# Optimization experiments

Hardware: AMD Instinct MI355X
Metric: run time of the kernel (lower is better)

The kernel has to match this reference:

```python
import jax, jax.numpy as jnp
import numpy as np
from jax import lax

FX, FY = 518.857, 519.469   # NYU-v2 depth intrinsics (cx/cy unused by forward)
B, H, W = 8, 479, 639       # TRAIN_CROP_SIZE = [W, H]; H+1, W+1 divisible by 4
P = 8                       # even PATCH_SIZE -> box-filter output is [H+1, W+1]
EPS = 1e-6


def _coords():
    # u_u0 = x - W/2, v_v0 = y - H/2, broadcast over [B,1,H,W]
    u = jnp.arange(W, dtype=jnp.float32)[None, None, None, :] - W / 2.0
    v = jnp.arange(H, dtype=jnp.float32)[None, None, :, None] - H / 2.0
    return u, v


def _surface_normal(xyz):
    # xyz: [H, W, 3] -> normals [H, W, 3]
    x, y, z = xyz[..., 0], xyz[..., 1], xyz[..., 2]
    # 9 box-filtered moments in a single depthwise conv (the original does 9 conv2d calls)
    mom = jnp.stack([x * x, x * y, x * z, y * y, y * z, z * z, x, y, z], 0)[None]  # [1,9,H,W]
    kern = jnp.ones((9, 1, P, P), xyz.dtype)
    s = lax.conv_general_dilated(mom, kern, (1, 1), [(P // 2, P // 2)] * 2,
                                 feature_group_count=9)[0]  # [9, H+1, W+1]
    xx, xy, xz, yy, yz, zz, xs, ys, zs = s
    ATA = jnp.stack([xx, xy, xz, xy, yy, yz, xz, yz, zz], -1)  # [H+1, W+1, 9]
    Hp, Wp = ATA.shape[0], ATA.shape[1]
    ATA = ATA.reshape(Hp, Wp, 3, 3) + EPS * jnp.eye(3, dtype=xyz.dtype)
    AT1 = jnp.stack([xs, ys, zs], -1)[..., None]  # [H+1, W+1, 3, 1]
    # original loops over 4x4 sub-patches with overlap=0 -> equivalent full-grid solve
    n = jnp.linalg.solve(ATA, AT1)                # [H+1, W+1, 3, 1]
    n = n / jnp.sqrt(jnp.sum(n * n, axis=2, keepdims=True))
    n = n[:-1, :-1, :, 0]                         # [H, W, 3]
    # orient toward camera: flip where dot(n, xyz) > 0
    flip = jnp.sum(n * xyz, axis=2, keepdims=True) > 0
    return jnp.where(flip, -n, n)


def _fit_normals(depth):
    # depth: [B,1,H,W] -> surface normals [B,3,H,W], zeroed where depth <= 0
    u, v = _coords()
    x = u * depth / FX
    y = v * depth / FY
    xyz = jnp.concatenate([x, y, depth], 1).transpose(0, 2, 3, 1)  # [B,H,W,3]
    sn = jax.vmap(_surface_normal)(xyz).transpose(0, 3, 1, 2)      # [B,3,H,W]
    return jnp.where(depth > 0, sn, 0.0)


def setup_inputs() -> dict:
    key = jax.random.key(0)
    k1, k2 = jax.random.split(key)
    prediction = jax.random.uniform(k1, (B, 1, H, W), jnp.float32)
    gt = jax.random.uniform(k2, (B, 1, H, W), jnp.float32)
    return {"prediction": prediction, "gt": gt}


def reference(prediction, gt):
    return jnp.mean(jnp.abs(_fit_normals(prediction) - _fit_normals(gt)))
```

## Files before the change

kernel.cpp:

```cpp
#include <hip/hip_runtime.h>

#define HH 479
#define WW 639
#define BATCH 8
#define NBLK (20 * 30 * 8)


__device__ __forceinline__ void solve_normal(
    float xx, float xy, float xz, float yy, float yz, float zz,
    float xs, float ys, float zs,
    float a_c, float b_c, float d0,
    float* nx, float* ny, float* nz)
{
    const float EPSV = 1e-6f;
    const float inv64 = 1.0f / 64.0f;
    float hx = xs * inv64, hy = ys * inv64, hz = zs * inv64;
    float cxx = fmaf(-hx, xs, xx) + EPSV;
    float cxy = fmaf(-hx, ys, xy);
    float cxz = fmaf(-hx, zs, xz);
    float cyy = fmaf(-hy, ys, yy) + EPSV;
    float cyz = fmaf(-hy, zs, yz);
    float czz = fmaf(-hz, zs, zz) + EPSV;
    float c00 = fmaf(cyy, czz, -cyz * cyz);
    float c01 = fmaf(cxz, cyz, -cxy * czz);
    float c02 = fmaf(cxy, cyz, -cxz * cyy);
    float c11 = fmaf(cxx, czz, -cxz * cxz);
    float c12 = fmaf(cxy, cxz, -cxx * cyz);
    float c22 = fmaf(cxx, cyy, -cxy * cxy);
    float m0 = fmaf(c00, xs, fmaf(c01, ys, c02 * zs));
    float m1 = fmaf(c01, xs, fmaf(c11, ys, c12 * zs));
    float m2 = fmaf(c02, xs, fmaf(c12, ys, c22 * zs));
    float g  = fmaf(m0, a_c, fmaf(m1, b_c, m2));
    float inv = rsqrtf(fmaf(m0, m0, fmaf(m1, m1, m2 * m2)));
    if (g > 0.0f) inv = -inv;
    if (!(d0 > 0.0f)) inv = 0.0f;
    *nx = m0 * inv; *ny = m1 * inv; *nz = m2 * inv;
}

__global__ __launch_bounds__(256, 8)
void ppal_main(const float* __restrict__ pred, const float* __restrict__ gt,
               double* __restrict__ acc)
{
    const int tx = threadIdx.x;
    const int ty = threadIdx.y;
    const int tid = ty * 16 + tx;
    const int j0 = blockIdx.x * 32;
    const int i0 = blockIdx.y * 16;
    const int b  = blockIdx.z;

    const float invFX = 1.0f / 518.857f;
    const float invFY = 1.0f / 519.469f;

    __shared__ float sd[2][23 * 41];
    __shared__ float4 cs4[624];
    __shared__ float  csTb[624];
    __shared__ float  wsum[4];

    const float* src0 = pred + (size_t)b * (HH * WW);
    const float* src1 = gt   + (size_t)b * (HH * WW);
    for (int idx = tid; idx < 23 * 41; idx += 256) {
        int lr = idx / 41, lc = idx - lr * 41;
        int r = i0 - 4 + lr, c = j0 - 4 + lc;
        bool ok = (lc < 39) && (r >= 0) && (r < HH) && (c >= 0) && (c < WW);
        int off = r * WW + c;
        sd[0][idx] = ok ? src0[off] : 0.0f;
        sd[1][idx] = ok ? src1[off] : 0.0f;
    }

    float aw[9];
#pragma unroll
    for (int m = 0; m < 9; ++m)
        aw[m] = ((float)(j0 + 2 * tx + m - 4) - 319.5f) * invFX;
    const float bc = ((float)(i0 + ty) - 239.5f) * invFY;
    const int ebase = ty * 39 + 2 * tx;

    float n0A[3], n1A[3];
    float contrib = 0.0f;

    __syncthreads();

#pragma unroll
    for (int k = 0; k < 2; ++k) {
        if (tid < 156) {
            int g = tid / 39;
            int c = tid - 39 * g;
            int rb = 4 * g;
            const float* col = &sd[k][c];
            float bv = ((float)(i0 + rb - 4) - 239.5f) * invFY;
            float S1 = 0.f, Sb = 0.f, Sbb = 0.f, T1 = 0.f, Tb = 0.f;
#pragma unroll
            for (int r = 0; r < 8; ++r) {
                float d  = col[(rb + r) * 41];
                float bvr = fmaf((float)r, invFY, bv);
                float bd = bvr * d;
                T1 += d;  Tb += bd;
                S1  = fmaf(d,  d,  S1);
                Sb  = fmaf(bd, d,  Sb);
                Sbb = fmaf(bd, bd, Sbb);
            }
            int e = rb * 39 + c;
            cs4[e]  = make_float4(S1, Sb, Sbb, T1);
            csTb[e] = Tb;
#pragma unroll
            for (int s = 1; s < 4; ++s) {
                float d0 = col[(rb + s - 1) * 41];
                float d1 = col[(rb + s + 7) * 41];
                float b0 = fmaf((float)(s - 1), invFY, bv);
                float b1 = fmaf((float)(s + 7), invFY, bv);
                float bd0 = b0 * d0, bd1 = b1 * d1;
                T1 += d1 - d0;
                Tb += bd1 - bd0;
                S1  += fmaf(d1,  d1,  -d0  * d0);
                Sb  += fmaf(bd1, d1,  -bd0 * d0);
                Sbb += fmaf(bd1, bd1, -bd0 * bd0);
                e += 39;
                cs4[e]  = make_float4(S1, Sb, Sbb, T1);
                csTb[e] = Tb;
            }
        }
        __syncthreads();

        {
            float Sxx = 0.f, Sxy = 0.f, Sxz = 0.f, Syy = 0.f, Syz = 0.f;
            float Szz = 0.f, Sxs = 0.f, Sys = 0.f, Szs = 0.f;
#pragma unroll
            for (int m = 1; m < 8; ++m) {
                int e = ebase + m;
                float4 r = cs4[e];
                float  tb = csTb[e];
                Szz += r.x;  Syz += r.y;  Syy += r.z;
                Szs += r.w;  Sys += tb;
                Sxz = fmaf(aw[m],         r.x, Sxz);
                Sxy = fmaf(aw[m],         r.y, Sxy);
                Sxs = fmaf(aw[m],         r.w, Sxs);
                Sxx = fmaf(aw[m] * aw[m], r.x, Sxx);
            }

            float nn[2][3];
#pragma unroll
            for (int p = 0; p < 2; ++p) {
                int m = (p == 0) ? 0 : 8;
                int e = ebase + m;
                float4 r = cs4[e];
                float  tb = csTb[e];
                float xx = fmaf(aw[m] * aw[m], r.x, Sxx);
                float xy = fmaf(aw[m], r.y, Sxy);
                float xz = fmaf(aw[m], r.x, Sxz);
                float yy = Syy + r.z;
                float yz = Syz + r.y;
                float zz = Szz + r.x;
                float xs = fmaf(aw[m], r.w, Sxs);
                float ys = Sys + tb;
                float zs = Szs + r.w;
                float d0 = sd[k][(ty + 4) * 41 + (2 * tx + p + 4)];
                solve_normal(xx, xy, xz, yy, yz, zz, xs, ys, zs,
                             aw[4 + p], bc, d0, &nn[p][0], &nn[p][1], &nn[p][2]);
            }
            if (k == 0) {
                n0A[0] = nn[0][0]; n0A[1] = nn[0][1]; n0A[2] = nn[0][2];
                n1A[0] = nn[1][0]; n1A[1] = nn[1][1]; n1A[2] = nn[1][2];
                __syncthreads();
            } else {
                const int i = i0 + ty;
                const bool valid0 = (i < HH);
                const bool valid1 = (i < HH) && (j0 + 2 * tx + 1 < WW);
                float c0 = fabsf(n0A[0] - nn[0][0]) + fabsf(n0A[1] - nn[0][1])
                         + fabsf(n0A[2] - nn[0][2]);
                float c1 = fabsf(n1A[0] - nn[1][0]) + fabsf(n1A[1] - nn[1][1])
                         + fabsf(n1A[2] - nn[1][2]);
                contrib = (valid0 ? c0 : 0.0f) + (valid1 ? c1 : 0.0f);
            }
        }
    }

    float v = contrib;
#pragma unroll
    for (int off = 32; off > 0; off >>= 1) v += __shfl_down(v, off, 64);
    int wid = tid >> 6, lane = tid & 63;
    if (lane == 0) wsum[wid] = v;
    __syncthreads();
    if (tid == 0) {
        double bs = (double)wsum[0] + (double)wsum[1] + (double)wsum[2] + (double)wsum[3];
        int slot = blockIdx.x + 20 * blockIdx.y + 600 * blockIdx.z;
        acc[slot] = bs;
    }
}

__global__ void ppal_finalize(const double* __restrict__ acc, float* __restrict__ out)
{
    int tid = threadIdx.x;
    double v = 0.0;
    for (int s = tid; s < NBLK; s += 256) v += acc[s];
#pragma unroll
    for (int off = 32; off > 0; off >>= 1) v += __shfl_down(v, off, 64);
    __shared__ double wsum[4];
    int wid = tid >> 6, lane = tid & 63;
    if (lane == 0) wsum[wid] = v;
    __syncthreads();
    if (tid == 0)
        out[0] = (float)((wsum[0] + wsum[1] + wsum[2] + wsum[3])
                         * (1.0 / 7345944.0));
}

extern "C" void kernel_launch(void* const* d_in, const int* in_sizes, int n_in,
                              void* d_out, int out_size, void* d_ws, size_t ws_size,
                              hipStream_t stream)
{
    const float* pred = (const float*)d_in[0];
    const float* gt   = (const float*)d_in[1];
    float* out  = (float*)d_out;
    double* acc = (double*)d_ws;

    dim3 grid(20, 30, BATCH);
    dim3 block(16, 16);
    ppal_main<<<grid, block, 0, stream>>>(pred, gt, acc);
    ppal_finalize<<<1, 256, 0, stream>>>(acc, out);
}
```

Measured before the change: 98.24 us.

## Process prediction and ground truth together with doubled shared buffers

```diff
diff --git a/kernel.cpp b/kernel.cpp
--- a/kernel.cpp
+++ b/kernel.cpp
@@ -37,7 +37,7 @@
     *nx = m0 * inv; *ny = m1 * inv; *nz = m2 * inv;
 }
 
-__global__ __launch_bounds__(256, 8)
+__global__ __launch_bounds__(256, 4)
 void ppal_main(const float* __restrict__ pred, const float* __restrict__ gt,
                double* __restrict__ acc)
 {
@@ -52,8 +52,8 @@
     const float invFY = 1.0f / 519.469f;
 
     __shared__ float sd[2][23 * 41];
-    __shared__ float4 cs4[624];
-    __shared__ float  csTb[624];
+    __shared__ float4 cs4[2][624];
+    __shared__ float  csTb[2][624];
     __shared__ float  wsum[4];
 
     const float* src0 = pred + (size_t)b * (HH * WW);
@@ -74,102 +74,127 @@
     const float bc = ((float)(i0 + ty) - 239.5f) * invFY;
     const int ebase = ty * 39 + 2 * tx;
 
-    float n0A[3], n1A[3];
+    __syncthreads();
+
+    if (tid < 156) {
+        int g = tid / 39;
+        int c = tid - 39 * g;
+        int rb = 4 * g;
+        const float* colA = &sd[0][c];
+        const float* colB = &sd[1][c];
+        float bv = ((float)(i0 + rb - 4) - 239.5f) * invFY;
+        float SA1 = 0.f, SAb = 0.f, SAbb = 0.f, TA1 = 0.f, TAb = 0.f;
+        float SB1 = 0.f, SBb = 0.f, SBbb = 0.f, TB1 = 0.f, TBb = 0.f;
+#pragma unroll
+        for (int r = 0; r < 8; ++r) {
+            int ro = (rb + r) * 41;
+            float bvr = fmaf((float)r, invFY, bv);
+            float dA = colA[ro], dB = colB[ro];
+            float bdA = bvr * dA, bdB = bvr * dB;
+            TA1 += dA;  TAb += bdA;
+            SA1  = fmaf(dA,  dA,  SA1);
+            SAb  = fmaf(bdA, dA,  SAb);
+            SAbb = fmaf(bdA, bdA, SAbb);
+            TB1 += dB;  TBb += bdB;
+            SB1  = fmaf(dB,  dB,  SB1);
+            SBb  = fmaf(bdB, dB,  SBb);
+            SBbb = fmaf(bdB, bdB, SBbb);
+        }
+        int e = rb * 39 + c;
+        cs4[0][e]  = make_float4(SA1, SAb, SAbb, TA1);
+        csTb[0][e] = TAb;
+        cs4[1][e]  = make_float4(SB1, SBb, SBbb, TB1);
+        csTb[1][e] = TBb;
+#pragma unroll
+        for (int s = 1; s < 4; ++s) {
+            int o0 = (rb + s - 1) * 41, o1 = (rb + s + 7) * 41;
+            float b0 = fmaf((float)(s - 1), invFY, bv);
+            float b1 = fmaf((float)(s + 7), invFY, bv);
+            float d0A = colA[o0], d1A = colA[o1];
+            float d0B = colB[o0], d1B = colB[o1];
+            float bd0A = b0 * d0A, bd1A = b1 * d1A;
+            float bd0B = b0 * d0B, bd1B = b1 * d1B;
+            TA1 += d1A - d0A;
+            TAb += bd1A - bd0A;
+            SA1  += fmaf(d1A,  d1A,  -d0A  * d0A);
+            SAb  += fmaf(bd1A, d1A,  -bd0A * d0A);
+            SAbb += fmaf(bd1A, bd1A, -bd0A * bd0A);
+            TB1 += d1B - d0B;
+            TBb += bd1B - bd0B;
+            SB1  += fmaf(d1B,  d1B,  -d0B  * d0B);
+            SBb  += fmaf(bd1B, d1B,  -bd0B * d0B);
+            SBbb += fmaf(bd1B, bd1B, -bd0B * bd0B);
+            e += 39;
+            cs4[0][e]  = make_float4(SA1, SAb, SAbb, TA1);
+            csTb[0][e] = TAb;
+            cs4[1][e]  = make_float4(SB1, SBb, SBbb, TB1);
+            csTb[1][e] = TBb;
+        }
+    }
+    __syncthreads();
+
     float contrib = 0.0f;
-
-    __syncthreads();
-
-#pragma unroll
-    for (int k = 0; k < 2; ++k) {
-        if (tid < 156) {
-            int g = tid / 39;
-            int c = tid - 39 * g;
-            int rb = 4 * g;
-            const float* col = &sd[k][c];
-            float bv = ((float)(i0 + rb - 4) - 239.5f) * invFY;
-            float S1 = 0.f, Sb = 0.f, Sbb = 0.f, T1 = 0.f, Tb = 0.f;
-#pragma unroll
-            for (int r = 0; r < 8; ++r) {
-                float d  = col[(rb + r) * 41];
-                float bvr = fmaf((float)r, invFY, bv);
-                float bd = bvr * d;
-                T1 += d;  Tb += bd;
-                S1  = fmaf(d,  d,  S1);
-                Sb  = fmaf(bd, d,  Sb);
-                Sbb = fmaf(bd, bd, Sbb);
-            }
-            int e = rb * 39 + c;
-            cs4[e]  = make_float4(S1, Sb, Sbb, T1);
-            csTb[e] = Tb;
-#pragma unroll
-            for (int s = 1; s < 4; ++s) {
-                float d0 = col[(rb + s - 1) * 41];
-                float d1 = col[(rb + s + 7) * 41];
-                float b0 = fmaf((float)(s - 1), invFY, bv);
-                float b1 = fmaf((float)(s + 7), invFY, bv);
-                float bd0 = b0 * d0, bd1 = b1 * d1;
-                T1 += d1 - d0;
-                Tb += bd1 - bd0;
-                S1  += fmaf(d1,  d1,  -d0  * d0);
-                Sb  += fmaf(bd1, d1,  -bd0 * d0);
-                Sbb += fmaf(bd1, bd1, -bd0 * bd0);
-                e += 39;
-                cs4[e]  = make_float4(S1, Sb, Sbb, T1);
-                csTb[e] = Tb;
-            }
-        }
-        __syncthreads();
-
-        {
-            float Sxx = 0.f, Sxy = 0.f, Sxz = 0.f, Syy = 0.f, Syz = 0.f;
-            float Szz = 0.f, Sxs = 0.f, Sys = 0.f, Szs = 0.f;
-#pragma unroll
-            for (int m = 1; m < 8; ++m) {
-                int e = ebase + m;
-                float4 r = cs4[e];
-                float  tb = csTb[e];
-                Szz += r.x;  Syz += r.y;  Syy += r.z;
-                Szs += r.w;  Sys += tb;
-                Sxz = fmaf(aw[m],         r.x, Sxz);
-                Sxy = fmaf(aw[m],         r.y, Sxy);
-                Sxs = fmaf(aw[m],         r.w, Sxs);
-                Sxx = fmaf(aw[m] * aw[m], r.x, Sxx);
-            }
-
-            float nn[2][3];
-#pragma unroll
-            for (int p = 0; p < 2; ++p) {
-                int m = (p == 0) ? 0 : 8;
-                int e = ebase + m;
-                float4 r = cs4[e];
-                float  tb = csTb[e];
-                float xx = fmaf(aw[m] * aw[m], r.x, Sxx);
-                float xy = fmaf(aw[m], r.y, Sxy);
-                float xz = fmaf(aw[m], r.x, Sxz);
-                float yy = Syy + r.z;
-                float yz = Syz + r.y;
-                float zz = Szz + r.x;
-                float xs = fmaf(aw[m], r.w, Sxs);
-                float ys = Sys + tb;
-                float zs = Szs + r.w;
-                float d0 = sd[k][(ty + 4) * 41 + (2 * tx + p + 4)];
-                solve_normal(xx, xy, xz, yy, yz, zz, xs, ys, zs,
-                             aw[4 + p], bc, d0, &nn[p][0], &nn[p][1], &nn[p][2]);
-            }
-            if (k == 0) {
-                n0A[0] = nn[0][0]; n0A[1] = nn[0][1]; n0A[2] = nn[0][2];
-                n1A[0] = nn[1][0]; n1A[1] = nn[1][1]; n1A[2] = nn[1][2];
-                __syncthreads();
-            } else {
-                const int i = i0 + ty;
-                const bool valid0 = (i < HH);
-                const bool valid1 = (i < HH) && (j0 + 2 * tx + 1 < WW);
-                float c0 = fabsf(n0A[0] - nn[0][0]) + fabsf(n0A[1] - nn[0][1])
-                         + fabsf(n0A[2] - nn[0][2]);
-                float c1 = fabsf(n1A[0] - nn[1][0]) + fabsf(n1A[1] - nn[1][1])
-                         + fabsf(n1A[2] - nn[1][2]);
-                contrib = (valid0 ? c0 : 0.0f) + (valid1 ? c1 : 0.0f);
-            }
+    {
+        float SxxA = 0.f, SxyA = 0.f, SxzA = 0.f, SyyA = 0.f, SyzA = 0.f;
+        float SzzA = 0.f, SxsA = 0.f, SysA = 0.f, SzsA = 0.f;
+        float SxxB = 0.f, SxyB = 0.f, SxzB = 0.f, SyyB = 0.f, SyzB = 0.f;
+        float SzzB = 0.f, SxsB = 0.f, SysB = 0.f, SzsB = 0.f;
+#pragma unroll
+        for (int m = 1; m < 8; ++m) {
+            int e = ebase + m;
+            float awm = aw[m], awm2 = awm * awm;
+            float4 rA = cs4[0][e];
+            float  tA = csTb[0][e];
+            float4 rB = cs4[1][e];
+            float  tB = csTb[1][e];
+            SzzA += rA.x;  SyzA += rA.y;  SyyA += rA.z;
+            SzsA += rA.w;  SysA += tA;
+            SxzA = fmaf(awm,  rA.x, SxzA);
+            SxyA = fmaf(awm,  rA.y, SxyA);
+            SxsA = fmaf(awm,  rA.w, SxsA);
+            SxxA = fmaf(awm2, rA.x, SxxA);
+            SzzB += rB.x;  SyzB += rB.y;  SyyB += rB.z;
+            SzsB += rB.w;  SysB += tB;
+            SxzB = fmaf(awm,  rB.x, SxzB);
+            SxyB = fmaf(awm,  rB.y, SxyB);
+            SxsB = fmaf(awm,  rB.w, SxsB);
+            SxxB = fmaf(awm2, rB.x, SxxB);
+        }
+
+        const int i = i0 + ty;
+        const bool valid0 = (i < HH);
+        const bool valid1 = (i < HH) && (j0 + 2 * tx + 1 < WW);
+#pragma unroll
+        for (int p = 0; p < 2; ++p) {
+            int m = (p == 0) ? 0 : 8;
+            int e = ebase + m;
+            float awm = aw[m], awm2 = awm * awm;
+            int doff = (ty + 4) * 41 + (2 * tx + p + 4);
+
+            float4 rA = cs4[0][e];
+            float  tA = csTb[0][e];
+            float nA[3];
+            solve_normal(fmaf(awm2, rA.x, SxxA), fmaf(awm, rA.y, SxyA),
+                         fmaf(awm, rA.x, SxzA),  SyyA + rA.z,
+                         SyzA + rA.y,            SzzA + rA.x,
+                         fmaf(awm, rA.w, SxsA),  SysA + tA,
+                         SzsA + rA.w,
+                         aw[4 + p], bc, sd[0][doff], &nA[0], &nA[1], &nA[2]);
+
+            float4 rB = cs4[1][e];
+            float  tB = csTb[1][e];
+            float nB[3];
+            solve_normal(fmaf(awm2, rB.x, SxxB), fmaf(awm, rB.y, SxyB),
+                         fmaf(awm, rB.x, SxzB),  SyyB + rB.z,
+                         SyzB + rB.y,            SzzB + rB.x,
+                         fmaf(awm, rB.w, SxsB),  SysB + tB,
+                         SzsB + rB.w,
+                         aw[4 + p], bc, sd[1][doff], &nB[0], &nB[1], &nB[2]);
+
+            float cp = fabsf(nA[0] - nB[0]) + fabsf(nA[1] - nB[1])
+                     + fabsf(nA[2] - nB[2]);
+            bool v = (p == 0) ? valid0 : valid1;
+            contrib += v ? cp : 0.0f;
         }
     }
 
```

New measurement: 102.3 us. 4.2% more time.
